# Performance work log

Measured on AMD Instinct MI355X. Metric: run time of the kernel, lower is better.

The kernel has to match this reference:

```python
import jax, jax.numpy as jnp
import numpy as np

N = 100000      # nodes
E = 300000      # directed edges (avg degree ~3, ogbn-arxiv-like sparsity)
F_IN = 128      # ogbn-arxiv node features
H = 256         # hidden
C = 40          # ogbn-arxiv classes
L = 6           # num_layers
BN_EPS = 1e-5


def setup_inputs() -> dict:
    key = jax.random.key(0)
    ks = jax.random.split(key, 12)
    x = jax.random.normal(ks[0], (N, F_IN), jnp.float32)
    edge_index = jax.random.randint(ks[1], (2, E), 0, N, dtype=jnp.int32)
    s_in = 1.0 / np.sqrt(F_IN)
    s_h = 1.0 / np.sqrt(H)
    return {
        "x": x,
        "edge_index": edge_index,
        "w_in": jax.random.normal(ks[2], (F_IN, H), jnp.float32) * s_in,
        "b_in": jnp.zeros((H,), jnp.float32),
        "conv_w": jax.random.normal(ks[3], (L, H, H), jnp.float32) * s_h,
        "conv_b": jnp.zeros((L, H), jnp.float32),
        "bn_gamma": jnp.ones((L, H), jnp.float32),
        "bn_beta": jnp.zeros((L, H), jnp.float32),
        "out_w": jax.random.normal(ks[4], (H, C), jnp.float32) * s_h,
        "out_b": jnp.zeros((C,), jnp.float32),
        "res_weights": jax.random.normal(ks[5], (L,), jnp.float32),
    }


def _gcn_norm(edge_index, n_nodes):
    # GCNConv default: add self-loops, symmetric normalization D^-1/2 (A+I) D^-1/2
    loops = jnp.arange(n_nodes, dtype=edge_index.dtype)
    src = jnp.concatenate([edge_index[0], loops])
    dst = jnp.concatenate([edge_index[1], loops])
    deg = jax.ops.segment_sum(jnp.ones_like(dst, jnp.float32), dst, num_segments=n_nodes)
    dinv = jax.lax.rsqrt(jnp.maximum(deg, 1.0))
    norm = dinv[src] * dinv[dst]  # [E+N]
    return src, dst, norm


def _batchnorm(h, gamma, beta):
    # BatchNorm1d in training mode: biased batch statistics over nodes
    m = jnp.mean(h, axis=0)
    v = jnp.mean(jnp.square(h - m), axis=0)
    return (h - m) * jax.lax.rsqrt(v + BN_EPS) * gamma + beta


def reference(x, edge_index, w_in, b_in, conv_w, conv_b, bn_gamma, bn_beta, out_w, out_b, res_weights):
    src, dst, norm = _gcn_norm(edge_index, N)
    h = x @ w_in + b_in            # input_fc: [N, H]
    x_input = h
    layer_out = []
    prev = None
    for i in range(L):
        hw = h @ conv_w[i]                                  # linear transform
        msg = hw[src] * norm[:, None]                       # gather + scale
        agg = jax.ops.segment_sum(msg, dst, num_segments=N) + conv_b[i]  # scatter-add
        a = jax.nn.relu(_batchnorm(agg, bn_gamma[i], bn_beta[i]))
        # dropout p=0.5 omitted (eval mode / deterministic reference)
        if i == 0:
            h = a + 0.2 * x_input
        else:
            h = a + 0.2 * x_input + 0.7 * prev
        layer_out.append(h)
        prev = h
    w = jax.nn.softmax(res_weights)                          # [L]
    mix = jnp.einsum('lnh,l->nh', jnp.stack(layer_out), w)   # weighted sum of layer outputs
    logits = mix @ out_w + out_b                             # [N, C]
    return jax.nn.log_softmax(logits, axis=1)
```

## Files before the change

### kernel.cpp

```cpp
#include <hip/hip_runtime.h>
#include <math.h>

#define Nn   100000
#define Ee   300000
#define FIN  128
#define Hdim 256
#define Ncls 40
#define Lnum 6
#define SCAN_B 98

typedef __attribute__((ext_vector_type(8))) short bf16x8;
typedef __attribute__((ext_vector_type(4))) float f32x4;

__device__ __forceinline__ float bf2f(unsigned int u16) {
    unsigned int x = u16 << 16;
    return __builtin_bit_cast(float, x);
}
__device__ __forceinline__ unsigned short f2bf(float f) {
    unsigned int x = __builtin_bit_cast(unsigned int, f);
    x = (x + 0x7FFFu + ((x >> 16) & 1u)) >> 16;
    return (unsigned short)x;
}
__device__ __forceinline__ void unpack2(unsigned int u, float& lo, float& hi) {
    lo = __builtin_bit_cast(float, u << 16);
    hi = __builtin_bit_cast(float, u & 0xFFFF0000u);
}
__device__ __forceinline__ unsigned int pack2(float a, float b) {
    return (unsigned int)f2bf(a) | ((unsigned int)f2bf(b) << 16);
}

__global__ void count_edges(const int* __restrict__ ei, int* __restrict__ cnt) {
    int e = blockIdx.x * blockDim.x + threadIdx.x;
    if (e < Ee) atomicAdd(&cnt[ei[Ee + e]], 1);
}

__global__ void scan_block(const int* __restrict__ cnt, int* __restrict__ iscan,
                           int* __restrict__ btot) {
    __shared__ int buf[1024];
    int t = threadIdx.x;
    int g = blockIdx.x * 1024 + t;
    int v = (g < Nn) ? cnt[g] : 0;
    buf[t] = v; __syncthreads();
    for (int off = 1; off < 1024; off <<= 1) {
        int x = buf[t];
        int a = (t >= off) ? buf[t - off] : 0;
        __syncthreads();
        buf[t] = x + a;
        __syncthreads();
    }
    if (g < Nn) iscan[g] = buf[t];
    if (t == 1023) btot[blockIdx.x] = buf[1023];
}

__global__ void scan_tops(const int* __restrict__ btot, int* __restrict__ bpref) {
    __shared__ int b[128];
    int t = threadIdx.x;
    int v = (t < SCAN_B) ? btot[t] : 0;
    b[t] = v; __syncthreads();
    for (int off = 1; off < 128; off <<= 1) {
        int x = b[t];
        int a = (t >= off) ? b[t - off] : 0;
        __syncthreads();
        b[t] = x + a;
        __syncthreads();
    }
    if (t < SCAN_B) bpref[t] = b[t] - v;
}

__global__ void scan_final(const int* __restrict__ cnt, const int* __restrict__ iscan,
                           const int* __restrict__ bpref, int* __restrict__ offs,
                           float* __restrict__ dinvp) {
    int g = blockIdx.x * 1024 + threadIdx.x;
    if (g < Nn) {
        int c = cnt[g];
        offs[g] = bpref[blockIdx.x] + iscan[g] - c;
        dinvp[g] = rsqrtf((float)(c + 1));
    }
    if (g == 0) offs[Nn] = Ee;
}

__global__ void fill_csr(const int* __restrict__ ei, const int* __restrict__ offs,
                         int* __restrict__ cur, const float* __restrict__ dinvp,
                         int* __restrict__ esrc, float* __restrict__ ew) {
    int e = blockIdx.x * blockDim.x + threadIdx.x;
    if (e >= Ee) return;
    int s = ei[e], d = ei[Ee + e];
    int p = offs[d] + atomicAdd(&cur[d], 1);
    esrc[p] = s;
    ew[p] = dinvp[s];
}

__global__ void prep_weights(const float* __restrict__ conv_w, const float* __restrict__ w_in,
                             const float* __restrict__ out_w,
                             unsigned short* __restrict__ Whi,
                             unsigned short* __restrict__ Fhi,
                             unsigned short* __restrict__ Whd, unsigned short* __restrict__ Wld) {
    int b = blockIdx.x, t = threadIdx.x;
    if (b < 1536) {
        int id = b * 256 + t;
        int l = id >> 16, k = (id >> 8) & 255, n = id & 255;
        Whi[l * 65536 + n * 256 + k] = f2bf(conv_w[id]);
    } else if (b < 1664) {
        int id = (b - 1536) * 256 + t;
        int k = id >> 8, n = id & 255;
        Fhi[n * FIN + k] = f2bf(w_in[id]);
    } else {
        int id = (b - 1664) * 256 + t;
        int c = id >> 8, k = id & 255;
        float w = (c < Ncls) ? out_w[k * Ncls + c] : 0.f;
        unsigned short hi = f2bf(w);
        unsigned short lo = f2bf(w - bf2f(hi));
        Whd[c * 256 + k] = hi;
        Wld[c * 256 + k] = lo;
    }
}

__global__ void cvt_bf16(const float* __restrict__ src, unsigned short* __restrict__ dst, int n8) {
    int i = blockIdx.x * blockDim.x + threadIdx.x;
    if (i >= n8) return;
    float4 a = ((const float4*)src)[i * 2];
    float4 b = ((const float4*)src)[i * 2 + 1];
    uint4 o;
    o.x = pack2(a.x, a.y); o.y = pack2(a.z, a.w);
    o.z = pack2(b.x, b.y); o.w = pack2(b.z, b.w);
    ((uint4*)dst)[i] = o;
}

__global__ void agg_kernel(const unsigned short* __restrict__ Hin,
                           unsigned short* __restrict__ T,
                           const int* __restrict__ offs, const int* __restrict__ esrc,
                           const float* __restrict__ ew, const float* __restrict__ dinvp,
                           float* __restrict__ bnsum, float* __restrict__ bnsq) {
    int t = threadIdx.x;
    if (blockIdx.x == 0) { bnsum[t] = 0.f; bnsq[t] = 0.f; }
    int wv = t >> 6, lane = t & 63;
    int n = blockIdx.x * 4 + wv;
    int o0 = offs[n], o1 = offs[n + 1];
    float dn = dinvp[n];
    uint2 u = *(const uint2*)&Hin[(size_t)n * Hdim + lane * 4];
    float a0, a1, a2, a3;
    unpack2(u.x, a0, a1); unpack2(u.y, a2, a3);
    a0 *= dn; a1 *= dn; a2 *= dn; a3 *= dn;
    for (int e = o0; e < o1; ++e) {
        int s = esrc[e];
        float w = ew[e];
        uint2 us = *(const uint2*)&Hin[(size_t)s * Hdim + lane * 4];
        float v0, v1, v2, v3;
        unpack2(us.x, v0, v1); unpack2(us.y, v2, v3);
        a0 += w * v0; a1 += w * v1; a2 += w * v2; a3 += w * v3;
    }
    uint2 o;
    o.x = pack2(dn * a0, dn * a1); o.y = pack2(dn * a2, dn * a3);
    *(uint2*)&T[(size_t)n * Hdim + lane * 4] = o;
}

__global__ void bn_reduce(const float* __restrict__ P, float* __restrict__ bnsum,
                          float* __restrict__ bnsq, int nb) {
    int c = threadIdx.x;
    int per = (nb + gridDim.x - 1) / gridDim.x;
    int r0 = blockIdx.x * per;
    int r1 = r0 + per; if (r1 > nb) r1 = nb;
    float s = 0.f, q = 0.f;
    for (int r = r0; r < r1; ++r) {
        s += P[(size_t)r * 512 + c];
        q += P[(size_t)r * 512 + 256 + c];
    }
    if (r0 < r1) {
        atomicAdd(&bnsum[c], s);
        atomicAdd(&bnsq[c], q);
    }
}

__global__ __launch_bounds__(512) void gemm_mfma(
    const unsigned short* __restrict__ A, unsigned short* __restrict__ C,
    const unsigned short* __restrict__ W,
    const float* __restrict__ bias, int K, int nrows,
    float* __restrict__ bnsum, float* __restrict__ bnsq, int do_stats,
    float* __restrict__ Pstats)
{
    __shared__ __align__(16) unsigned short smem[18432];
    __shared__ float lsum[256];
    __shared__ float lsq[256];

    const int t    = threadIdx.x;
    const int lane = t & 63, wid = t >> 6;
    const int ln   = lane & 15, quad = lane >> 4;
    const int r64  = (wid >> 2) * 64, c64 = (wid & 3) * 64;
    const int r0   = blockIdx.x * 128;

    if (t < 256) { lsum[t] = 0.f; lsq[t] = 0.f; }

    unsigned short* At = smem;
    unsigned short* Bt = smem + 5120;

    f32x4 acc[4][4];
#pragma unroll
    for (int i = 0; i < 4; ++i)
#pragma unroll
        for (int j = 0; j < 4; ++j) acc[i][j] = (f32x4){0.f, 0.f, 0.f, 0.f};

    const int arow = t >> 2, akq = t & 3;
    const bool arow_ok = (r0 + arow < nrows);
    const int nk = K >> 5;

    uint4 ga = make_uint4(0u, 0u, 0u, 0u);
    if (arow_ok) ga = *(const uint4*)&A[(size_t)(r0 + arow) * K + akq * 8];
    uint4 gb[2];
#pragma unroll
    for (int q = 0; q < 2; ++q) {
        int idx = t + 512 * q, row = idx >> 2, kq = idx & 3;
        gb[q] = *(const uint4*)&W[(size_t)row * K + kq * 8];
    }

    for (int kt = 0; kt < nk; ++kt) {
        __syncthreads();
        *(uint4*)&At[arow * 40 + akq * 8] = ga;
#pragma unroll
        for (int q = 0; q < 2; ++q) {
            int idx = t + 512 * q, row = idx >> 2, kq = idx & 3;
            *(uint4*)&Bt[row * 40 + kq * 8] = gb[q];
        }
        __syncthreads();
        if (kt + 1 < nk) {
            int k0 = (kt + 1) << 5;
            ga = make_uint4(0u, 0u, 0u, 0u);
            if (arow_ok) ga = *(const uint4*)&A[(size_t)(r0 + arow) * K + k0 + akq * 8];
#pragma unroll
            for (int q = 0; q < 2; ++q) {
                int idx = t + 512 * q, row = idx >> 2, kq = idx & 3;
                gb[q] = *(const uint4*)&W[(size_t)row * K + k0 + kq * 8];
            }
        }
        bf16x8 af[4], bf[4];
#pragma unroll
        for (int rt = 0; rt < 4; ++rt)
            af[rt] = *(const bf16x8*)&At[(r64 + rt * 16 + ln) * 40 + quad * 8];
#pragma unroll
        for (int ct = 0; ct < 4; ++ct)
            bf[ct] = *(const bf16x8*)&Bt[(c64 + ct * 16 + ln) * 40 + quad * 8];
#pragma unroll
        for (int rt = 0; rt < 4; ++rt)
#pragma unroll
            for (int ct = 0; ct < 4; ++ct)
                acc[rt][ct] = __builtin_amdgcn_mfma_f32_16x16x32_bf16(af[rt], bf[ct], acc[rt][ct], 0, 0, 0);
    }
    __syncthreads();

    float bc[4];
#pragma unroll
    for (int ct = 0; ct < 4; ++ct) bc[ct] = bias[c64 + ct * 16 + ln];

    if (do_stats) {
#pragma unroll
        for (int ct = 0; ct < 4; ++ct) {
            float s = 0.f, qq = 0.f;
#pragma unroll
            for (int rt = 0; rt < 4; ++rt)
#pragma unroll
                for (int v = 0; v < 4; ++v) {
                    int row = r0 + r64 + rt * 16 + quad * 4 + v;
                    if (row < nrows) {
                        float val = acc[rt][ct][v] + bc[ct];
                        s += val; qq += val * val;
                    }
                }
            s  += __shfl_xor(s, 16);  s  += __shfl_xor(s, 32);
            qq += __shfl_xor(qq, 16); qq += __shfl_xor(qq, 32);
            if (quad == 0) { atomicAdd(&lsum[c64 + ct * 16 + ln], s); atomicAdd(&lsq[c64 + ct * 16 + ln], qq); }
        }
    }

    unsigned short* Tt = &smem[wid * 2304];
    const int rr2 = lane & 31, jh = lane >> 5;
#pragma unroll
    for (int h = 0; h < 2; ++h) {
#pragma unroll
        for (int rr = 0; rr < 2; ++rr) {
            int rt = 2 * h + rr;
#pragma unroll
            for (int ct = 0; ct < 4; ++ct)
#pragma unroll
                for (int v = 0; v < 4; ++v)
                    Tt[(rr * 16 + quad * 4 + v) * 72 + ct * 16 + ln] = f2bf(acc[rt][ct][v] + bc[ct]);
        }
        __asm__ volatile("s_waitcnt lgkmcnt(0)" ::: "memory");
        int grow = r0 + r64 + h * 32 + rr2;
        if (grow < nrows) {
#pragma unroll
            for (int j = 0; j < 4; ++j) {
                uint4 v4 = *(const uint4*)&Tt[rr2 * 72 + jh * 32 + j * 8];
                *(uint4*)&C[(size_t)grow * 256 + c64 + jh * 32 + j * 8] = v4;
            }
        }
        __asm__ volatile("s_waitcnt lgkmcnt(0)" ::: "memory");
    }

    if (do_stats) {
        __syncthreads();
        if (t < 256) {
            if (Pstats) {
                Pstats[(size_t)blockIdx.x * 512 + t]       = lsum[t];
                Pstats[(size_t)blockIdx.x * 512 + 256 + t] = lsq[t];
            } else {
                atomicAdd(&bnsum[t], lsum[t]);
                atomicAdd(&bnsq[t], lsq[t]);
            }
        }
    }
}

__global__ void apply_kernel(const unsigned short* __restrict__ T,
                             const unsigned short* __restrict__ X,
                             unsigned short* __restrict__ Hb, unsigned short* __restrict__ M,
                             const float* __restrict__ bnsum, const float* __restrict__ bnsq,
                             const float* __restrict__ gamma, const float* __restrict__ beta,
                             const float* __restrict__ res_w, int layer) {
    __shared__ float sc[256], sh[256];
    int t = threadIdx.x;
    {
        float mean = bnsum[t] * (1.0f / Nn);
        float var  = fmaxf(bnsq[t] * (1.0f / Nn) - mean * mean, 0.f);
        float rstd = rsqrtf(var + 1e-5f);
        float s = gamma[t] * rstd;
        sc[t] = s; sh[t] = beta[t] - mean * s;
    }
    float m0 = res_w[0];
#pragma unroll
    for (int i = 1; i < Lnum; ++i) m0 = fmaxf(m0, res_w[i]);
    float se = 0.f, wl = 0.f;
#pragma unroll
    for (int i = 0; i < Lnum; ++i) {
        float e = __expf(res_w[i] - m0);
        se += e;
        if (i == layer) wl = e;
    }
    float wi = wl / se;
    __syncthreads();

    int idx = blockIdx.x * blockDim.x + t;
    int c8 = idx & 31;
    float scl[8], shl[8];
#pragma unroll
    for (int k = 0; k < 8; ++k) { scl[k] = sc[c8 * 8 + k]; shl[k] = sh[c8 * 8 + k]; }

    uint4 tv = ((const uint4*)T)[idx];
    uint4 xv = ((const uint4*)X)[idx];
    float tf[8], xf[8];
    unpack2(tv.x, tf[0], tf[1]); unpack2(tv.y, tf[2], tf[3]);
    unpack2(tv.z, tf[4], tf[5]); unpack2(tv.w, tf[6], tf[7]);
    unpack2(xv.x, xf[0], xf[1]); unpack2(xv.y, xf[2], xf[3]);
    unpack2(xv.z, xf[4], xf[5]); unpack2(xv.w, xf[6], xf[7]);

    float a[8];
#pragma unroll
    for (int k = 0; k < 8; ++k)
        a[k] = fmaxf(tf[k] * scl[k] + shl[k], 0.f) + 0.2f * xf[k];
    if (layer > 0) {
        uint4 hv = ((const uint4*)Hb)[idx];
        float hf[8];
        unpack2(hv.x, hf[0], hf[1]); unpack2(hv.y, hf[2], hf[3]);
        unpack2(hv.z, hf[4], hf[5]); unpack2(hv.w, hf[6], hf[7]);
#pragma unroll
        for (int k = 0; k < 8; ++k) a[k] += 0.7f * hf[k];
    }
    uint4 ho;
    ho.x = pack2(a[0], a[1]); ho.y = pack2(a[2], a[3]);
    ho.z = pack2(a[4], a[5]); ho.w = pack2(a[6], a[7]);
    ((uint4*)Hb)[idx] = ho;

    float m[8];
    if (layer == 0) {
#pragma unroll
        for (int k = 0; k < 8; ++k) m[k] = wi * a[k];
    } else {
        uint4 mv = ((const uint4*)M)[idx];
        float mf[8];
        unpack2(mv.x, mf[0], mf[1]); unpack2(mv.y, mf[2], mf[3]);
        unpack2(mv.z, mf[4], mf[5]); unpack2(mv.w, mf[6], mf[7]);
#pragma unroll
        for (int k = 0; k < 8; ++k) m[k] = mf[k] + wi * a[k];
    }
    uint4 mo;
    mo.x = pack2(m[0], m[1]); mo.y = pack2(m[2], m[3]);
    mo.z = pack2(m[4], m[5]); mo.w = pack2(m[6], m[7]);
    ((uint4*)M)[idx] = mo;
}

__global__ __launch_bounds__(512) void head_mfma(const unsigned short* __restrict__ M,
                                                 const unsigned short* __restrict__ Whd,
                                                 const unsigned short* __restrict__ Wld,
                                                 const float* __restrict__ out_b,
                                                 float* __restrict__ out, int nrows) {
    __shared__ unsigned short At[128 * 40];
    const int t    = threadIdx.x;
    const int lane = t & 63, wid = t >> 6;
    const int ln   = lane & 15, quad = lane >> 4;
    const int r0   = blockIdx.x * 128;

    f32x4 acc[3];
#pragma unroll
    for (int ct = 0; ct < 3; ++ct) acc[ct] = (f32x4){0.f, 0.f, 0.f, 0.f};

    for (int k0 = 0; k0 < 256; k0 += 32) {
        __syncthreads();
        {
            int row = t >> 2, kq = t & 3;
            uint4 g = make_uint4(0u, 0u, 0u, 0u);
            if (r0 + row < nrows)
                g = *(const uint4*)&M[(size_t)(r0 + row) * 256 + k0 + kq * 8];
            *(uint4*)&At[row * 40 + kq * 8] = g;
        }
        __syncthreads();
        bf16x8 af = *(const bf16x8*)&At[(wid * 16 + ln) * 40 + quad * 8];
#pragma unroll
        for (int ct = 0; ct < 3; ++ct) {
            int c = ct * 16 + ln;
            bf16x8 bh = *(const bf16x8*)&Whd[c * 256 + k0 + quad * 8];
            bf16x8 bl = *(const bf16x8*)&Wld[c * 256 + k0 + quad * 8];
            acc[ct] = __builtin_amdgcn_mfma_f32_16x16x32_bf16(af, bh, acc[ct], 0, 0, 0);
            acc[ct] = __builtin_amdgcn_mfma_f32_16x16x32_bf16(af, bl, acc[ct], 0, 0, 0);
        }
    }

    int   cc[3]; float bias[3];
#pragma unroll
    for (int ct = 0; ct < 3; ++ct) {
        cc[ct] = ct * 16 + ln;
        bias[ct] = (cc[ct] < Ncls) ? out_b[cc[ct]] : 0.f;
    }
#pragma unroll
    for (int v = 0; v < 4; ++v) {
        int row = r0 + wid * 16 + quad * 4 + v;
        float val[3];
#pragma unroll
        for (int ct = 0; ct < 3; ++ct) val[ct] = acc[ct][v] + bias[ct];
        float mx = -1e30f;
#pragma unroll
        for (int ct = 0; ct < 3; ++ct) if (cc[ct] < Ncls) mx = fmaxf(mx, val[ct]);
        mx = fmaxf(mx, __shfl_xor(mx, 1)); mx = fmaxf(mx, __shfl_xor(mx, 2));
        mx = fmaxf(mx, __shfl_xor(mx, 4)); mx = fmaxf(mx, __shfl_xor(mx, 8));
        float s = 0.f;
#pragma unroll
        for (int ct = 0; ct < 3; ++ct) if (cc[ct] < Ncls) s += __expf(val[ct] - mx);
        s += __shfl_xor(s, 1); s += __shfl_xor(s, 2);
        s += __shfl_xor(s, 4); s += __shfl_xor(s, 8);
        float lse = mx + __logf(s);
        if (row < nrows) {
            out[(size_t)row * Ncls + cc[0]] = val[0] - lse;
            out[(size_t)row * Ncls + cc[1]] = val[1] - lse;
            if (ln < 8) out[(size_t)row * Ncls + cc[2]] = val[2] - lse;
        }
    }
}

extern "C" void kernel_launch(void* const* d_in, const int* in_sizes, int n_in,
                              void* d_out, int out_size, void* d_ws, size_t ws_size,
                              hipStream_t stream)
{
    const float* x      = (const float*)d_in[0];
    const int*   ei     = (const int*)d_in[1];
    const float* w_in   = (const float*)d_in[2];
    const float* b_in   = (const float*)d_in[3];
    const float* conv_w = (const float*)d_in[4];
    const float* conv_b = (const float*)d_in[5];
    const float* gamma  = (const float*)d_in[6];
    const float* beta   = (const float*)d_in[7];
    const float* out_w  = (const float*)d_in[8];
    const float* out_b  = (const float*)d_in[9];
    const float* res_w  = (const float*)d_in[10];
    float* out = (float*)d_out;
    char* ws = (char*)d_ws;

    int*   cnt    = (int*)  (ws + 0);
    int*   cursor = (int*)  (ws + 400000);
    int*   offs   = (int*)  (ws + 800000);
    float* dinvp  = (float*)(ws + 1200016);
    int*   esrc   = (int*)  (ws + 1600016);
    float* ew     = (float*)(ws + 2800016);
    float* bnsum  = (float*)(ws + 4000016);
    float* bnsq   = (float*)(ws + 4001040);
    int*   iscan  = (int*)  (ws + 4002064);
    int*   btot   = (int*)  (ws + 4402064);
    int*   bpref  = (int*)  (ws + 4402576);
    unsigned short* Whi = (unsigned short*)(ws + 4403088);
    unsigned short* Fhi = (unsigned short*)(ws + 5975952);
    unsigned short* Whd = (unsigned short*)(ws + 6107024);
    unsigned short* Wld = (unsigned short*)(ws + 6131600);
    unsigned short* X   = (unsigned short*)(ws + 6156176);
    unsigned short* Hb  = X  + (size_t)Nn * Hdim;
    unsigned short* T   = Hb + (size_t)Nn * Hdim;
    unsigned short* M   = T  + (size_t)Nn * Hdim;
    unsigned short* xbf = M;

    const int gblocks = (Nn + 127) / 128;

    const size_t P_OFS = 6156176 + 4 * (size_t)Nn * Hdim * sizeof(unsigned short);
    const size_t P_BYTES = (size_t)gblocks * 512 * sizeof(float);
    float* Pst = (ws_size >= P_OFS + P_BYTES) ? (float*)(ws + P_OFS) : nullptr;

    hipMemsetAsync(cnt, 0, 800000, stream);

    count_edges<<<(Ee + 255) / 256, 256, 0, stream>>>(ei, cnt);
    scan_block<<<SCAN_B, 1024, 0, stream>>>(cnt, iscan, btot);
    scan_tops<<<1, 128, 0, stream>>>(btot, bpref);
    scan_final<<<SCAN_B, 1024, 0, stream>>>(cnt, iscan, bpref, offs, dinvp);
    fill_csr<<<(Ee + 255) / 256, 256, 0, stream>>>(ei, offs, cursor, dinvp, esrc, ew);

    prep_weights<<<1712, 256, 0, stream>>>(conv_w, w_in, out_w,
                                           Whi, Fhi, Whd, Wld);
    cvt_bf16<<<(Nn * FIN / 8 + 255) / 256, 256, 0, stream>>>(x, xbf, Nn * FIN / 8);

    gemm_mfma<<<gblocks, 512, 0, stream>>>(xbf, X, Fhi, b_in, FIN, Nn,
                                           nullptr, nullptr, 0, nullptr);

    for (int i = 0; i < Lnum; ++i) {
        agg_kernel<<<Nn / 4, 256, 0, stream>>>(i == 0 ? X : Hb, T, offs, esrc, ew, dinvp,
                                               bnsum, bnsq);
        gemm_mfma<<<gblocks, 512, 0, stream>>>(T, T,
                                               Whi + (size_t)i * Hdim * Hdim,
                                               conv_b + (size_t)i * Hdim,
                                               Hdim, Nn, bnsum, bnsq, 1, Pst);
        if (Pst)
            bn_reduce<<<64, 256, 0, stream>>>(Pst, bnsum, bnsq, gblocks);
        apply_kernel<<<(Nn * 32) / 256, 256, 0, stream>>>(T, X, Hb, M,
                                                          bnsum, bnsq,
                                                          gamma + (size_t)i * Hdim,
                                                          beta + (size_t)i * Hdim,
                                                          res_w, i);
    }

    head_mfma<<<gblocks, 512, 0, stream>>>(M, Whd, Wld, out_b, out, Nn);
}
```

Measured before the change: 1.263 ms.

## Fuse conv GEMM, BatchNorm reduction and residual apply into cooperative kernel

Replaces the per-layer gemm + bn_reduce + apply sequence with one cooperative kernel. It computes the GEMM tile in registers, writes per-block BN partials, reduces them across the grid with grid syncs, then applies BN, ReLU, the residual and the mix straight from the accumulators. This removes the write and re-read of the GEMM output T and two launches per layer. In exchange it needs all blocks resident at once (gblocks ~782 blocks of 512 threads), reuses T as partial-sum scratch, and falls back to the old path if the cooperative launch fails.

```diff
diff --git a/kernel.cpp b/kernel.cpp
--- a/kernel.cpp
+++ b/kernel.cpp
@@ -1,5 +1,8 @@
 #include <hip/hip_runtime.h>
+#include <hip/hip_cooperative_groups.h>
 #include <math.h>
+
+namespace cg = cooperative_groups;
 
 #define Nn   100000
 #define Ee   300000
@@ -309,6 +312,223 @@
     }
 }
 
+__global__ __launch_bounds__(512, 8) void gemm_apply(
+    const unsigned short* A,
+    const unsigned short* __restrict__ W,
+    const float* __restrict__ bias,
+    const unsigned short* __restrict__ X,
+    unsigned short* __restrict__ Hb,
+    unsigned short* __restrict__ Mb,
+    float* Pscratch,
+    float* __restrict__ bnsum, float* __restrict__ bnsq,
+    const float* __restrict__ gammaL, const float* __restrict__ betaL,
+    const float* __restrict__ res_w, int layer)
+{
+    __shared__ __align__(16) unsigned short smem[18432];
+    __shared__ float lsum[256];
+    __shared__ float lsq[256];
+
+    const int t    = threadIdx.x;
+    const int lane = t & 63, wid = t >> 6;
+    const int ln   = lane & 15, quad = lane >> 4;
+    const int r64  = (wid >> 2) * 64, c64 = (wid & 3) * 64;
+    const int bid  = blockIdx.x;
+    const int r0   = bid * 128;
+
+    if (t < 256) { lsum[t] = 0.f; lsq[t] = 0.f; }
+
+    unsigned short* At = smem;
+    unsigned short* Bt = smem + 5120;
+
+    f32x4 acc[4][4];
+#pragma unroll
+    for (int i = 0; i < 4; ++i)
+#pragma unroll
+        for (int j = 0; j < 4; ++j) acc[i][j] = (f32x4){0.f, 0.f, 0.f, 0.f};
+
+    const int K = Hdim, nk = Hdim >> 5;
+    const int arow = t >> 2, akq = t & 3;
+    const bool arow_ok = (r0 + arow < Nn);
+
+    uint4 ga = make_uint4(0u, 0u, 0u, 0u);
+    if (arow_ok) ga = *(const uint4*)&A[(size_t)(r0 + arow) * K + akq * 8];
+    uint4 gb[2];
+#pragma unroll
+    for (int q = 0; q < 2; ++q) {
+        int idx = t + 512 * q, row = idx >> 2, kq = idx & 3;
+        gb[q] = *(const uint4*)&W[(size_t)row * K + kq * 8];
+    }
+
+    for (int kt = 0; kt < nk; ++kt) {
+        __syncthreads();
+        *(uint4*)&At[arow * 40 + akq * 8] = ga;
+#pragma unroll
+        for (int q = 0; q < 2; ++q) {
+            int idx = t + 512 * q, row = idx >> 2, kq = idx & 3;
+            *(uint4*)&Bt[row * 40 + kq * 8] = gb[q];
+        }
+        __syncthreads();
+        if (kt + 1 < nk) {
+            int k0 = (kt + 1) << 5;
+            ga = make_uint4(0u, 0u, 0u, 0u);
+            if (arow_ok) ga = *(const uint4*)&A[(size_t)(r0 + arow) * K + k0 + akq * 8];
+#pragma unroll
+            for (int q = 0; q < 2; ++q) {
+                int idx = t + 512 * q, row = idx >> 2, kq = idx & 3;
+                gb[q] = *(const uint4*)&W[(size_t)row * K + k0 + kq * 8];
+            }
+        }
+        bf16x8 af[4], bf[4];
+#pragma unroll
+        for (int rt = 0; rt < 4; ++rt)
+            af[rt] = *(const bf16x8*)&At[(r64 + rt * 16 + ln) * 40 + quad * 8];
+#pragma unroll
+        for (int ct = 0; ct < 4; ++ct)
+            bf[ct] = *(const bf16x8*)&Bt[(c64 + ct * 16 + ln) * 40 + quad * 8];
+#pragma unroll
+        for (int rt = 0; rt < 4; ++rt)
+#pragma unroll
+            for (int ct = 0; ct < 4; ++ct)
+                acc[rt][ct] = __builtin_amdgcn_mfma_f32_16x16x32_bf16(af[rt], bf[ct], acc[rt][ct], 0, 0, 0);
+    }
+    __syncthreads();
+
+    float bc[4];
+#pragma unroll
+    for (int ct = 0; ct < 4; ++ct) bc[ct] = bias[c64 + ct * 16 + ln];
+
+#pragma unroll
+    for (int ct = 0; ct < 4; ++ct) {
+        float s = 0.f, qq = 0.f;
+#pragma unroll
+        for (int rt = 0; rt < 4; ++rt)
+#pragma unroll
+            for (int v = 0; v < 4; ++v) {
+                int row = r0 + r64 + rt * 16 + quad * 4 + v;
+                if (row < Nn) {
+                    float val = acc[rt][ct][v] + bc[ct];
+                    s += val; qq += val * val;
+                }
+            }
+        s  += __shfl_xor(s, 16);  s  += __shfl_xor(s, 32);
+        qq += __shfl_xor(qq, 16); qq += __shfl_xor(qq, 32);
+        if (quad == 0) { atomicAdd(&lsum[c64 + ct * 16 + ln], s); atomicAdd(&lsq[c64 + ct * 16 + ln], qq); }
+    }
+    __syncthreads();
+    if (t < 256) {
+        Pscratch[(size_t)bid * 16384 + t]       = lsum[t];
+        Pscratch[(size_t)bid * 16384 + 256 + t] = lsq[t];
+    }
+
+    cg::this_grid().sync();
+
+    if (bid < 512) {
+        const int kind = bid >> 8, c = bid & 255;
+        const int off = kind * 256 + c;
+        float s = 0.f;
+        for (int r = t; r < (int)gridDim.x; r += 512)
+            s += Pscratch[(size_t)r * 16384 + off];
+        float* red = (float*)smem;
+        red[t] = s;
+        __syncthreads();
+        for (int o = 256; o >= 1; o >>= 1) {
+            if (t < o) red[t] += red[t + o];
+            __syncthreads();
+        }
+        if (t == 0) { if (kind) bnsq[c] = red[0]; else bnsum[c] = red[0]; }
+    }
+
+    cg::this_grid().sync();
+
+    const float inv_n = 1.0f / (float)Nn;
+    float scv[4], shv[4];
+#pragma unroll
+    for (int ct = 0; ct < 4; ++ct) {
+        int ch = c64 + ct * 16 + ln;
+        float mean = bnsum[ch] * inv_n;
+        float var  = fmaxf(bnsq[ch] * inv_n - mean * mean, 0.f);
+        float rstd = rsqrtf(var + 1e-5f);
+        float s = gammaL[ch] * rstd;
+        scv[ct] = s; shv[ct] = betaL[ch] - mean * s;
+    }
+    float m0 = res_w[0];
+#pragma unroll
+    for (int i = 1; i < Lnum; ++i) m0 = fmaxf(m0, res_w[i]);
+    float se = 0.f, wl = 0.f;
+#pragma unroll
+    for (int i = 0; i < Lnum; ++i) {
+        float e = __expf(res_w[i] - m0);
+        se += e; if (i == layer) wl = e;
+    }
+    const float wi = wl / se;
+
+    const int l31 = lane & 31, lh = lane >> 5;
+#pragma unroll
+    for (int h = 0; h < 2; ++h) {
+        __syncthreads();
+        if ((wid >> 2) == h) {
+#pragma unroll
+            for (int rt = 0; rt < 4; ++rt)
+#pragma unroll
+                for (int ct = 0; ct < 4; ++ct)
+#pragma unroll
+                    for (int v = 0; v < 4; ++v) {
+                        float val = acc[rt][ct][v] + bc[ct];
+                        float a = fmaxf(val * scv[ct] + shv[ct], 0.f);
+                        smem[(rt * 16 + quad * 4 + v) * 268 + c64 + ct * 16 + ln] = f2bf(a);
+                    }
+        }
+        __syncthreads();
+#pragma unroll
+        for (int j = 0; j < 4; ++j) {
+            int rl = wid * 8 + 2 * j + lh;
+            int grow = r0 + h * 64 + rl;
+            uint4 av = *(const uint4*)&smem[rl * 268 + l31 * 8];
+            if (grow < Nn) {
+                size_t gbi = (size_t)grow * 256 + l31 * 8;
+                uint4 xv = *(const uint4*)&X[gbi];
+                float af_[8], xf[8];
+                unpack2(av.x, af_[0], af_[1]); unpack2(av.y, af_[2], af_[3]);
+                unpack2(av.z, af_[4], af_[5]); unpack2(av.w, af_[6], af_[7]);
+                unpack2(xv.x, xf[0], xf[1]); unpack2(xv.y, xf[2], xf[3]);
+                unpack2(xv.z, xf[4], xf[5]); unpack2(xv.w, xf[6], xf[7]);
+                float hn[8];
+                if (layer > 0) {
+                    uint4 hv = *(const uint4*)&Hb[gbi];
+                    float hf[8];
+                    unpack2(hv.x, hf[0], hf[1]); unpack2(hv.y, hf[2], hf[3]);
+                    unpack2(hv.z, hf[4], hf[5]); unpack2(hv.w, hf[6], hf[7]);
+#pragma unroll
+                    for (int k = 0; k < 8; ++k) hn[k] = af_[k] + 0.2f * xf[k] + 0.7f * hf[k];
+                } else {
+#pragma unroll
+                    for (int k = 0; k < 8; ++k) hn[k] = af_[k] + 0.2f * xf[k];
+                }
+                uint4 ho;
+                ho.x = pack2(hn[0], hn[1]); ho.y = pack2(hn[2], hn[3]);
+                ho.z = pack2(hn[4], hn[5]); ho.w = pack2(hn[6], hn[7]);
+                *(uint4*)&Hb[gbi] = ho;
+                float mm[8];
+                if (layer > 0) {
+                    uint4 mv = *(const uint4*)&Mb[gbi];
+                    float mf[8];
+                    unpack2(mv.x, mf[0], mf[1]); unpack2(mv.y, mf[2], mf[3]);
+                    unpack2(mv.z, mf[4], mf[5]); unpack2(mv.w, mf[6], mf[7]);
+#pragma unroll
+                    for (int k = 0; k < 8; ++k) mm[k] = mf[k] + wi * hn[k];
+                } else {
+#pragma unroll
+                    for (int k = 0; k < 8; ++k) mm[k] = wi * hn[k];
+                }
+                uint4 mo;
+                mo.x = pack2(mm[0], mm[1]); mo.y = pack2(mm[2], mm[3]);
+                mo.z = pack2(mm[4], mm[5]); mo.w = pack2(mm[6], mm[7]);
+                *(uint4*)&Mb[gbi] = mo;
+            }
+        }
+    }
+}
+
 __global__ void apply_kernel(const unsigned short* __restrict__ T,
                              const unsigned short* __restrict__ X,
                              unsigned short* __restrict__ Hb, unsigned short* __restrict__ M,
@@ -513,20 +733,46 @@
     gemm_mfma<<<gblocks, 512, 0, stream>>>(xbf, X, Fhi, b_in, FIN, Nn,
                                            nullptr, nullptr, 0, nullptr);
 
+    bool coop_ok = true;
     for (int i = 0; i < Lnum; ++i) {
         agg_kernel<<<Nn / 4, 256, 0, stream>>>(i == 0 ? X : Hb, T, offs, esrc, ew, dinvp,
                                                bnsum, bnsq);
-        gemm_mfma<<<gblocks, 512, 0, stream>>>(T, T,
-                                               Whi + (size_t)i * Hdim * Hdim,
-                                               conv_b + (size_t)i * Hdim,
-                                               Hdim, Nn, bnsum, bnsq, 1, Pst);
-        if (Pst)
-            bn_reduce<<<64, 256, 0, stream>>>(Pst, bnsum, bnsq, gblocks);
-        apply_kernel<<<(Nn * 32) / 256, 256, 0, stream>>>(T, X, Hb, M,
-                                                          bnsum, bnsq,
-                                                          gamma + (size_t)i * Hdim,
-                                                          beta + (size_t)i * Hdim,
-                                                          res_w, i);
+        if (coop_ok) {
+            const unsigned short* A_  = T;
+            const unsigned short* W_  = Whi + (size_t)i * Hdim * Hdim;
+            const float*          b_  = conv_b + (size_t)i * Hdim;
+            const unsigned short* X_  = X;
+            unsigned short*       H_  = Hb;
+            unsigned short*       M_  = M;
+            float*                Ps_ = (float*)T;
+            float*                bs_ = bnsum;
+            float*                bq_ = bnsq;
+            const float*          g_  = gamma + (size_t)i * Hdim;
+            const float*          be_ = beta  + (size_t)i * Hdim;
+            const float*          rw_ = res_w;
+            int                   li  = i;
+            void* kargs[] = { (void*)&A_, (void*)&W_, (void*)&b_, (void*)&X_,
+                              (void*)&H_, (void*)&M_, (void*)&Ps_, (void*)&bs_,
+                              (void*)&bq_, (void*)&g_, (void*)&be_, (void*)&rw_,
+                              (void*)&li };
+            hipError_t e = hipLaunchCooperativeKernel((const void*)gemm_apply,
+                                                      dim3(gblocks), dim3(512),
+                                                      kargs, 0, stream);
+            if (e != hipSuccess) coop_ok = false;
+        }
+        if (!coop_ok) {
+            gemm_mfma<<<gblocks, 512, 0, stream>>>(T, T,
+                                                   Whi + (size_t)i * Hdim * Hdim,
+                                                   conv_b + (size_t)i * Hdim,
+                                                   Hdim, Nn, bnsum, bnsq, 1, Pst);
+            if (Pst)
+                bn_reduce<<<64, 256, 0, stream>>>(Pst, bnsum, bnsq, gblocks);
+            apply_kernel<<<(Nn * 32) / 256, 256, 0, stream>>>(T, X, Hb, M,
+                                                              bnsum, bnsq,
+                                                              gamma + (size_t)i * Hdim,
+                                                              beta + (size_t)i * Hdim,
+                                                              res_w, i);
+        }
     }
 
     head_mfma<<<gblocks, 512, 0, stream>>>(M, Whd, Wld, out_b, out, Nn);
```

Measured after the change: 4.021 ms. +218.3%, slower.

## Fuse neighbor aggregation into the per-layer MFMA GEMM via shared-memory tile

Applied to the files above, without the earlier changes.

Replaces the separate aggregation kernel and the per-layer GEMM with one kernel. Each block aggregates its 128 rows of neighbor features straight into a padded LDS tile, then runs bf16 MFMA against weights read directly from global memory, and emits batch-norm partial stats. This removes the write and re-read of the aggregated tensor through HBM and one launch per layer. In exchange, the gather phase runs only 8 waves per block with a large LDS footprint, which may limit occupancy and latency hiding. It also adds a memset per layer to zero the stats.

```diff
diff --git a/kernel.cpp b/kernel.cpp
--- a/kernel.cpp
+++ b/kernel.cpp
@@ -8,6 +8,7 @@
 #define Ncls 40
 #define Lnum 6
 #define SCAN_B 98
+#define KP   264
 
 typedef __attribute__((ext_vector_type(8))) short bf16x8;
 typedef __attribute__((ext_vector_type(4))) float f32x4;
@@ -126,34 +127,6 @@
     ((uint4*)dst)[i] = o;
 }
 
-__global__ void agg_kernel(const unsigned short* __restrict__ Hin,
-                           unsigned short* __restrict__ T,
-                           const int* __restrict__ offs, const int* __restrict__ esrc,
-                           const float* __restrict__ ew, const float* __restrict__ dinvp,
-                           float* __restrict__ bnsum, float* __restrict__ bnsq) {
-    int t = threadIdx.x;
-    if (blockIdx.x == 0) { bnsum[t] = 0.f; bnsq[t] = 0.f; }
-    int wv = t >> 6, lane = t & 63;
-    int n = blockIdx.x * 4 + wv;
-    int o0 = offs[n], o1 = offs[n + 1];
-    float dn = dinvp[n];
-    uint2 u = *(const uint2*)&Hin[(size_t)n * Hdim + lane * 4];
-    float a0, a1, a2, a3;
-    unpack2(u.x, a0, a1); unpack2(u.y, a2, a3);
-    a0 *= dn; a1 *= dn; a2 *= dn; a3 *= dn;
-    for (int e = o0; e < o1; ++e) {
-        int s = esrc[e];
-        float w = ew[e];
-        uint2 us = *(const uint2*)&Hin[(size_t)s * Hdim + lane * 4];
-        float v0, v1, v2, v3;
-        unpack2(us.x, v0, v1); unpack2(us.y, v2, v3);
-        a0 += w * v0; a1 += w * v1; a2 += w * v2; a3 += w * v3;
-    }
-    uint2 o;
-    o.x = pack2(dn * a0, dn * a1); o.y = pack2(dn * a2, dn * a3);
-    *(uint2*)&T[(size_t)n * Hdim + lane * 4] = o;
-}
-
 __global__ void bn_reduce(const float* __restrict__ P, float* __restrict__ bnsum,
                           float* __restrict__ bnsq, int nb) {
     int c = threadIdx.x;
@@ -174,13 +147,9 @@
 __global__ __launch_bounds__(512) void gemm_mfma(
     const unsigned short* __restrict__ A, unsigned short* __restrict__ C,
     const unsigned short* __restrict__ W,
-    const float* __restrict__ bias, int K, int nrows,
-    float* __restrict__ bnsum, float* __restrict__ bnsq, int do_stats,
-    float* __restrict__ Pstats)
+    const float* __restrict__ bias, int K, int nrows)
 {
     __shared__ __align__(16) unsigned short smem[18432];
-    __shared__ float lsum[256];
-    __shared__ float lsq[256];
 
     const int t    = threadIdx.x;
     const int lane = t & 63, wid = t >> 6;
@@ -188,8 +157,6 @@
     const int r64  = (wid >> 2) * 64, c64 = (wid & 3) * 64;
     const int r0   = blockIdx.x * 128;
 
-    if (t < 256) { lsum[t] = 0.f; lsq[t] = 0.f; }
-
     unsigned short* At = smem;
     unsigned short* Bt = smem + 5120;
 
@@ -250,26 +217,6 @@
 #pragma unroll
     for (int ct = 0; ct < 4; ++ct) bc[ct] = bias[c64 + ct * 16 + ln];
 
-    if (do_stats) {
-#pragma unroll
-        for (int ct = 0; ct < 4; ++ct) {
-            float s = 0.f, qq = 0.f;
-#pragma unroll
-            for (int rt = 0; rt < 4; ++rt)
-#pragma unroll
-                for (int v = 0; v < 4; ++v) {
-                    int row = r0 + r64 + rt * 16 + quad * 4 + v;
-                    if (row < nrows) {
-                        float val = acc[rt][ct][v] + bc[ct];
-                        s += val; qq += val * val;
-                    }
-                }
-            s  += __shfl_xor(s, 16);  s  += __shfl_xor(s, 32);
-            qq += __shfl_xor(qq, 16); qq += __shfl_xor(qq, 32);
-            if (quad == 0) { atomicAdd(&lsum[c64 + ct * 16 + ln], s); atomicAdd(&lsq[c64 + ct * 16 + ln], qq); }
-        }
-    }
-
     unsigned short* Tt = &smem[wid * 2304];
     const int rr2 = lane & 31, jh = lane >> 5;
 #pragma unroll
@@ -294,17 +241,128 @@
         }
         __asm__ volatile("s_waitcnt lgkmcnt(0)" ::: "memory");
     }
-
-    if (do_stats) {
-        __syncthreads();
-        if (t < 256) {
-            if (Pstats) {
-                Pstats[(size_t)blockIdx.x * 512 + t]       = lsum[t];
-                Pstats[(size_t)blockIdx.x * 512 + 256 + t] = lsq[t];
-            } else {
-                atomicAdd(&bnsum[t], lsum[t]);
-                atomicAdd(&bnsq[t], lsq[t]);
+}
+
+__global__ __launch_bounds__(512, 4) void gemm_agg(
+    const unsigned short* __restrict__ Hin,
+    unsigned short* __restrict__ C,
+    const unsigned short* __restrict__ W,
+    const float* __restrict__ bias,
+    const int* __restrict__ offs, const int* __restrict__ esrc,
+    const float* __restrict__ ew, const float* __restrict__ dinvp,
+    float* __restrict__ bnsum, float* __restrict__ bnsq,
+    float* __restrict__ Pstats)
+{
+    __shared__ __align__(16) unsigned short At[128 * KP];
+    __shared__ float lsum[256], lsq[256];
+
+    const int t    = threadIdx.x;
+    const int lane = t & 63, wid = t >> 6;
+    const int ln   = lane & 15, quad = lane >> 4;
+    const int r64  = (wid >> 2) * 64, c64 = (wid & 3) * 64;
+    const int r0   = blockIdx.x * 128;
+
+    if (t < 256) { lsum[t] = 0.f; lsq[t] = 0.f; }
+
+    for (int rr = 0; rr < 16; ++rr) {
+        int lrow = wid * 16 + rr;
+        int n = r0 + lrow;
+        float a0 = 0.f, a1 = 0.f, a2 = 0.f, a3 = 0.f;
+        if (n < Nn) {
+            int o0 = offs[n], o1 = offs[n + 1];
+            float dn = dinvp[n];
+            uint2 u = *(const uint2*)&Hin[(size_t)n * Hdim + lane * 4];
+            unpack2(u.x, a0, a1); unpack2(u.y, a2, a3);
+            a0 *= dn; a1 *= dn; a2 *= dn; a3 *= dn;
+            for (int e = o0; e < o1; ++e) {
+                int s = esrc[e];
+                float w = ew[e];
+                uint2 us = *(const uint2*)&Hin[(size_t)s * Hdim + lane * 4];
+                float v0, v1, v2, v3;
+                unpack2(us.x, v0, v1); unpack2(us.y, v2, v3);
+                a0 += w * v0; a1 += w * v1; a2 += w * v2; a3 += w * v3;
             }
+            a0 *= dn; a1 *= dn; a2 *= dn; a3 *= dn;
+        }
+        *(uint2*)&At[lrow * KP + lane * 4] =
+            make_uint2(pack2(a0, a1), pack2(a2, a3));
+    }
+    __syncthreads();
+
+    f32x4 acc[4][4];
+#pragma unroll
+    for (int i = 0; i < 4; ++i)
+#pragma unroll
+        for (int j = 0; j < 4; ++j) acc[i][j] = (f32x4){0.f, 0.f, 0.f, 0.f};
+
+#pragma unroll
+    for (int kt = 0; kt < 8; ++kt) {
+        bf16x8 af[4], bf[4];
+#pragma unroll
+        for (int ct = 0; ct < 4; ++ct)
+            bf[ct] = *(const bf16x8*)&W[(size_t)(c64 + ct * 16 + ln) * 256 + kt * 32 + quad * 8];
+#pragma unroll
+        for (int rt = 0; rt < 4; ++rt)
+            af[rt] = *(const bf16x8*)&At[(r64 + rt * 16 + ln) * KP + kt * 32 + quad * 8];
+#pragma unroll
+        for (int rt = 0; rt < 4; ++rt)
+#pragma unroll
+            for (int ct = 0; ct < 4; ++ct)
+                acc[rt][ct] = __builtin_amdgcn_mfma_f32_16x16x32_bf16(af[rt], bf[ct], acc[rt][ct], 0, 0, 0);
+    }
+
+    float bc[4];
+#pragma unroll
+    for (int ct = 0; ct < 4; ++ct) bc[ct] = bias[c64 + ct * 16 + ln];
+
+#pragma unroll
+    for (int ct = 0; ct < 4; ++ct) {
+        float s = 0.f, qq = 0.f;
+#pragma unroll
+        for (int rt = 0; rt < 4; ++rt)
+#pragma unroll
+            for (int v = 0; v < 4; ++v) {
+                int row = r0 + r64 + rt * 16 + quad * 4 + v;
+                if (row < Nn) {
+                    float val = acc[rt][ct][v] + bc[ct];
+                    s += val; qq += val * val;
+                }
+            }
+        s  += __shfl_xor(s, 16);  s  += __shfl_xor(s, 32);
+        qq += __shfl_xor(qq, 16); qq += __shfl_xor(qq, 32);
+        if (quad == 0) { atomicAdd(&lsum[c64 + ct * 16 + ln], s); atomicAdd(&lsq[c64 + ct * 16 + ln], qq); }
+    }
+
+    __syncthreads();
+
+#pragma unroll
+    for (int rt = 0; rt < 4; ++rt)
+#pragma unroll
+        for (int ct = 0; ct < 4; ++ct)
+#pragma unroll
+            for (int v = 0; v < 4; ++v)
+                At[(r64 + rt * 16 + quad * 4 + v) * KP + c64 + ct * 16 + ln] =
+                    f2bf(acc[rt][ct][v] + bc[ct]);
+    __syncthreads();
+
+    const int l31 = t & 31, rhalf = t >> 5;
+#pragma unroll
+    for (int p = 0; p < 8; ++p) {
+        int lrow = p * 16 + rhalf;
+        int grow = r0 + lrow;
+        if (grow < Nn) {
+            uint4 v4 = *(const uint4*)&At[lrow * KP + l31 * 8];
+            *(uint4*)&C[(size_t)grow * 256 + l31 * 8] = v4;
+        }
+    }
+
+    if (t < 256) {
+        if (Pstats) {
+            Pstats[(size_t)blockIdx.x * 512 + t]       = lsum[t];
+            Pstats[(size_t)blockIdx.x * 512 + 256 + t] = lsq[t];
+        } else {
+            atomicAdd(&bnsum[t], lsum[t]);
+            atomicAdd(&bnsq[t], lsq[t]);
         }
     }
 }
@@ -510,16 +568,15 @@
                                            Whi, Fhi, Whd, Wld);
     cvt_bf16<<<(Nn * FIN / 8 + 255) / 256, 256, 0, stream>>>(x, xbf, Nn * FIN / 8);
 
-    gemm_mfma<<<gblocks, 512, 0, stream>>>(xbf, X, Fhi, b_in, FIN, Nn,
-                                           nullptr, nullptr, 0, nullptr);
+    gemm_mfma<<<gblocks, 512, 0, stream>>>(xbf, X, Fhi, b_in, FIN, Nn);
 
     for (int i = 0; i < Lnum; ++i) {
-        agg_kernel<<<Nn / 4, 256, 0, stream>>>(i == 0 ? X : Hb, T, offs, esrc, ew, dinvp,
-                                               bnsum, bnsq);
-        gemm_mfma<<<gblocks, 512, 0, stream>>>(T, T,
-                                               Whi + (size_t)i * Hdim * Hdim,
-                                               conv_b + (size_t)i * Hdim,
-                                               Hdim, Nn, bnsum, bnsq, 1, Pst);
+        hipMemsetAsync(bnsum, 0, 2048, stream);
+        gemm_agg<<<gblocks, 512, 0, stream>>>(i == 0 ? X : Hb, T,
+                                              Whi + (size_t)i * Hdim * Hdim,
+                                              conv_b + (size_t)i * Hdim,
+                                              offs, esrc, ew, dinvp,
+                                              bnsum, bnsq, Pst);
         if (Pst)
             bn_reduce<<<64, 256, 0, stream>>>(Pst, bnsum, bnsq, gblocks);
         apply_kernel<<<(Nn * 32) / 256, 256, 0, stream>>>(T, X, Hb, M,
```

New measurement: 1.316 ms. +4.2%, slower.
